# Optimization experiments

Hardware: AMD Instinct MI355X
Metric: run time of the kernel (lower is better)

The kernel has to match this reference:

```python
import jax, jax.numpy as jnp
import numpy as np
from functools import partial

DN = ('NCHW', 'OIHW', 'NCHW')

def _conv(x, w):
    # 'same' conv, stride 1, NCHW
    return jax.lax.conv_general_dilated(x, w, window_strides=(1, 1),
                                        padding='SAME', dimension_numbers=DN)

def setup_inputs() -> dict:
    key = jax.random.key(0)
    ks = jax.random.split(key, 5)
    B, T, Cin, Oh, H, Wd = 8, 16, 64, 64, 56, 56
    x = jax.random.normal(ks[0], (B, T, Cin, H, Wd), dtype=jnp.float32)
    h = jax.random.normal(ks[1], (B, Oh, H, Wd), dtype=jnp.float32)
    # xavier-uniform-ish init scale for 3x3 kernels
    def xavier(k, shape):
        fan_in = shape[1] * shape[2] * shape[3]
        fan_out = shape[0] * shape[2] * shape[3]
        a = float(np.sqrt(6.0 / (fan_in + fan_out)))
        return jax.random.uniform(k, shape, dtype=jnp.float32, minval=-a, maxval=a)
    W = xavier(ks[2], (3 * Oh, Cin, 3, 3))  # [Wz; Wr; Wc]
    U = xavier(ks[3], (2 * Oh, Oh, 3, 3))   # [Uz; Ur]
    C = xavier(ks[4], (Oh, Oh, 3, 3))       # Uc (on r*h)
    return {"x": x, "h": h, "W": W, "U": U, "C": C}

def reference(x, h, W, U, C):
    Oh = C.shape[0]
    xt_major = jnp.swapaxes(x, 0, 1)  # [T, B, Cin, H, W]

    def step(h, xt):
        wx = _conv(xt, W)             # [B, 3*Oh, H, W]
        uh = _conv(h, U)              # [B, 2*Oh, H, W]
        z = jax.nn.sigmoid(wx[:, :Oh] + uh[:, :Oh])            # update gate
        r = jax.nn.sigmoid(wx[:, Oh:2 * Oh] + uh[:, Oh:2 * Oh])  # reset gate
        h_tilde = jnp.tanh(wx[:, 2 * Oh:] + _conv(r * h, C))
        h_new = (1.0 - z) * h + z * h_tilde
        return h_new, h_new

    h_last, outs = jax.lax.scan(step, h, xt_major)
    return jnp.swapaxes(outs, 0, 1), h_last  # [B, T, Oh, H, W], [B, Oh, H, W]
```

## Files before the change

kernel.cpp:

```cpp
#include <hip/hip_runtime.h>
#include <math.h>


#define PIX 4224
#define PIMG 244992
#define BIMG ((size_t)8 * PIMG)
#define HL_OFF ((size_t)25690112)
#define SLOT 2176

typedef unsigned short u16;
typedef __attribute__((ext_vector_type(8))) __bf16 bf16x8;
typedef __attribute__((ext_vector_type(4))) float f32x4;

__device__ __forceinline__ float bf2f(u16 u) {
  unsigned v = ((unsigned)u) << 16;
  float f;
  __builtin_memcpy(&f, &v, 4);
  return f;
}
__device__ __forceinline__ u16 f2bf(float f) {
  unsigned u;
  __builtin_memcpy(&u, &f, 4);
  u = (u + 0x7FFFu + ((u >> 16) & 1u)) >> 16;
  return (u16)u;
}
__device__ __forceinline__ void gll16(const u16* g, u16* l) {
  __builtin_amdgcn_global_load_lds(
      (const __attribute__((address_space(1))) void*)g,
      (__attribute__((address_space(3))) void*)l, 16, 0, 0);
}

__device__ __forceinline__ void stage_row(const u16* img, int prow, int x0,
                                          u16* ring, int slot, int lane,
                                          int wv) {
  const u16* g = img + (size_t)prow * PIX + x0 * 64;
  u16* l = ring + slot * SLOT;
  gll16(g + wv * 512 + lane * 8, l + wv * 512);
  if (wv == 0 && lane < 16) gll16(g + 2048 + lane * 8, l + 2048);
}

__device__ __forceinline__ void loadB18(const u16* wr, int NCH,
                                        bf16x8 (&B)[6][3]) {
#pragma unroll
  for (int p = 0; p < 6; ++p) {
    const int ky = p >> 1, kc = p & 1;
#pragma unroll
    for (int kx = 0; kx < 3; ++kx)
      B[p][kx] = *(const bf16x8*)(wr + (size_t)((ky * 3 + kx) * NCH) * 64 +
                                  kc * 32);
  }
}

__device__ __forceinline__ void conv_unit(const u16* ring, int rcb,
                                          const bf16x8 (&B)[6][3],
                                          f32x4 (&acc)[2], int lane) {
#pragma unroll
  for (int p = 0; p < 6; ++p) {
    const int ky = p >> 1, kc = p & 1;
    const int slot = (rcb + ky) & 7;
    bf16x8 af[2][3];
#pragma unroll
    for (int mf = 0; mf < 2; ++mf)
#pragma unroll
      for (int kx = 0; kx < 3; ++kx) {
        const int pp = mf * 16 + (lane & 15) + kx;
        const int sl = (kc * 4 + (lane >> 4)) ^ (pp & 7);
        af[mf][kx] = *(const bf16x8*)(ring + slot * SLOT + pp * 64 + sl * 8);
      }
#pragma unroll
    for (int kx = 0; kx < 3; ++kx)
#pragma unroll
      for (int mf = 0; mf < 2; ++mf)
        acc[mf] = __builtin_amdgcn_mfma_f32_16x16x32_bf16(af[mf][kx], B[p][kx],
                                                          acc[mf], 0, 0, 0);
  }
}

#define UNIT_SYNC() \
  asm volatile("s_waitcnt vmcnt(0)" ::: "memory"); \
  __syncthreads();

__global__ __launch_bounds__(256) void wprep_k(const float* __restrict__ W,
                                               const float* __restrict__ U,
                                               const float* __restrict__ C,
                                               u16* __restrict__ wcat) {
  int i = blockIdx.x * 256 + threadIdx.x;
  if (i >= 221184) return;
  float v;
  if (i < 110592) {
    int plane = i / 12288, rem = i % 12288, o = rem / 64, ci = rem % 64;
    v = W[(size_t)(o * 64 + ci) * 9 + plane];
  } else if (i < 184320) {
    int j = i - 110592;
    int plane = j / 8192, rem = j % 8192, o = rem / 64, ci = rem % 64;
    v = U[(size_t)(o * 64 + ci) * 9 + plane];
  } else {
    int j = i - 184320;
    int plane = j / 4096, rem = j % 4096, o = rem / 64, ci = rem % 64;
    v = C[(size_t)(o * 64 + ci) * 9 + plane];
  }
  wcat[i] = f2bf(v);
}

__global__ __launch_bounds__(256) void hinit_k(const float* __restrict__ h,
                                               u16* __restrict__ hpad,
                                               float* __restrict__ hstate) {
  __shared__ float t[64][57];
  const int y = blockIdx.x, b = blockIdx.y;
  const int tid = threadIdx.x;
  for (int i = tid; i < 64 * 56; i += 256) {
    int ci = i / 56, xx = i % 56;
    t[ci][xx] = h[((size_t)(b * 64) + ci) * 3136 + y * 56 + xx];
  }
  __syncthreads();
  const size_t pb = (size_t)b * PIMG + (size_t)(y + 1) * PIX;
  const size_t sb = ((size_t)(b * 56) + y) * 64;
  for (int i = tid; i < 56 * 64; i += 256) {
    int px = i / 64, ci = i % 64;
    float v = t[ci][px];
    int gx = px + 1;
    hpad[pb + gx * 64 + (((ci >> 3) ^ (gx & 7)) << 3) + (ci & 7)] = f2bf(v);
    hstate[(sb + px) * 64 + ci] = v;
  }
}

__global__ __launch_bounds__(256) void xprep4_k(const float* __restrict__ x,
                                                u16* __restrict__ xring,
                                                int t0) {
  __shared__ float tt[64][57];
  const int y = blockIdx.x, b = blockIdx.y, t = t0 + blockIdx.z;
  const int tid = threadIdx.x;
  for (int i = tid; i < 64 * 56; i += 256) {
    int ci = i / 56, px = i % 56;
    tt[ci][px] = x[((size_t)(b * 16 + t) * 64 + ci) * 3136 + y * 56 + px];
  }
  __syncthreads();
  const size_t pb =
      (size_t)(t & 3) * BIMG + (size_t)b * PIMG + (size_t)(y + 1) * PIX;
  for (int i = tid; i < 56 * 64; i += 256) {
    int px = i / 64, ci = i % 64;
    int gx = px + 1;
    xring[pb + gx * 64 + (((ci >> 3) ^ (gx & 7)) << 3) + (ci & 7)] =
        f2bf(tt[ci][px]);
  }
}

__global__ __launch_bounds__(256, 3) void convW_k(const u16* __restrict__ xring,
                                                  const u16* __restrict__ wcat,
                                                  u16* __restrict__ wx) {
  __shared__ __align__(16) u16 ring[8 * SLOT];
  const int bid = blockIdx.x;
  const int ns = bid / 224;
  const int rem = bid % 224;
  const int b = rem & 7;
  const int r2 = rem >> 3;
  const int x0 = (r2 & 1) * 32;
  const int y0 = (r2 >> 1) * 4;
  const int lane = threadIdx.x & 63, wv = threadIdx.x >> 6;
  const int n0 = ns * 64 + wv * 16;

  const u16* wr = wcat + (size_t)(n0 + (lane & 15)) * 64 + (lane >> 4) * 8;
  bf16x8 B[6][3];
  loadB18(wr, 192, B);

  const u16* img0 = xring + (size_t)b * PIMG;

#pragma unroll
  for (int k = 0; k < 3; ++k)
    stage_row(img0, y0 + k, x0, ring, k, lane, wv);

  int S = 3;
#pragma unroll
  for (int u = 0; u < 16; ++u) {
    const int tt = u >> 2, yi = u & 3;
    UNIT_SYNC();
    const int tgt = (u + 1 < 16) ? (((u + 1) >> 2) * 6 + ((u + 1) & 3) + 2) : 2;
#pragma unroll
    for (; S <= tgt; ++S)
      stage_row(img0 + (size_t)(S / 6) * BIMG, y0 + S % 6, x0, ring, S & 7,
                lane, wv);

    f32x4 acc[2] = {{0.f, 0.f, 0.f, 0.f}, {0.f, 0.f, 0.f, 0.f}};
    conv_unit(ring, tt * 6 + yi, B, acc, lane);

    const int y = y0 + yi;
    const size_t rowb = ((size_t)(b * 4 + tt) * 56 + y) * 64;
    const int n = n0 + (lane & 15);
#pragma unroll
    for (int mf = 0; mf < 2; ++mf)
#pragma unroll
      for (int r = 0; r < 4; ++r) {
        const int px = x0 + mf * 16 + 4 * (lane >> 4) + r;
        wx[(rowb + px) * 192 + n] = f2bf(acc[mf][r]);
      }
  }
}

__global__ __launch_bounds__(256, 3) void convU_k(
    const u16* __restrict__ hpad, const u16* __restrict__ ucat,
    const u16* __restrict__ wx, _Float16* __restrict__ zbuf,
    u16* __restrict__ rhpad, int t) {
  __shared__ __align__(16) u16 ring[8 * SLOT];
  const int bid = blockIdx.x;
  const int ns = bid / 224;
  const int rem = bid % 224;
  const int b = rem & 7;
  const int r2 = rem >> 3;
  const int x0 = (r2 & 1) * 32;
  const int y0 = (r2 >> 1) * 4;
  const int lane = threadIdx.x & 63, wv = threadIdx.x >> 6;
  const int n0 = ns * 64 + wv * 16;

  const u16* wr = ucat + (size_t)(n0 + (lane & 15)) * 64 + (lane >> 4) * 8;
  bf16x8 B[6][3];
  loadB18(wr, 128, B);

  const u16* img = hpad + (size_t)b * PIMG;
#pragma unroll
  for (int k = 0; k < 3; ++k) stage_row(img, y0 + k, x0, ring, k, lane, wv);

  const int slott = t & 3;
  int S = 3;
#pragma unroll
  for (int u = 0; u < 4; ++u) {
    UNIT_SYNC();
    const int tgt = (u + 1 < 4) ? (u + 3) : 2;
#pragma unroll
    for (; S <= tgt; ++S)
      stage_row(img, y0 + S, x0, ring, S & 7, lane, wv);

    f32x4 acc[2] = {{0.f, 0.f, 0.f, 0.f}, {0.f, 0.f, 0.f, 0.f}};
    conv_unit(ring, u, B, acc, lane);

    const int y = y0 + u;
    const size_t wrowb = ((size_t)(b * 4 + slott) * 56 + y) * 64;
    const size_t rowb = ((size_t)(b * 56) + y) * 64;
    const int n = n0 + (lane & 15);
#pragma unroll
    for (int mf = 0; mf < 2; ++mf)
#pragma unroll
      for (int r = 0; r < 4; ++r) {
        const int px = x0 + mf * 16 + 4 * (lane >> 4) + r;
        if (px < 56) {
          const float a = bf2f(wx[(wrowb + px) * 192 + n]) + acc[mf][r];
          const float s = 1.f / (1.f + __expf(-a));
          if (ns == 0) {
            zbuf[(rowb + px) * 64 + n] = (_Float16)s;
          } else {
            const int ci = n - 64;
            const int cp = mf * 16 + 4 * (lane >> 4) + r + 1;
            const int slotc = (u + 1) & 7;
            const float hv =
                bf2f(ring[slotc * SLOT + cp * 64 +
                          (((ci >> 3) ^ (cp & 7)) << 3) + (ci & 7)]);
            const int gx = px + 1;
            rhpad[(size_t)b * PIMG + (size_t)(y + 1) * PIX + gx * 64 +
                  (((ci >> 3) ^ (gx & 7)) << 3) + (ci & 7)] = f2bf(s * hv);
          }
        }
      }
  }
}

__global__ __launch_bounds__(256, 3) void convC_k(
    const u16* __restrict__ rhpad, const u16* __restrict__ ccat,
    const u16* __restrict__ wx, const _Float16* __restrict__ zbuf,
    float* __restrict__ hstate, u16* __restrict__ hpad,
    float* __restrict__ out, int t) {
  __shared__ __align__(16) u16 ring[8 * SLOT];
  __shared__ float ldt[4][16][33];
  const int bid = blockIdx.x;
  const int b = bid & 7;
  const int r2 = bid >> 3;
  const int x0 = (r2 & 1) * 32;
  const int y0 = (r2 >> 1) * 2;
  const int lane = threadIdx.x & 63, wv = threadIdx.x >> 6;
  const int n0 = wv * 16;

  const u16* wr = ccat + (size_t)(n0 + (lane & 15)) * 64 + (lane >> 4) * 8;
  bf16x8 B[6][3];
  loadB18(wr, 64, B);

  const u16* img = rhpad + (size_t)b * PIMG;
#pragma unroll
  for (int k = 0; k < 3; ++k) stage_row(img, y0 + k, x0, ring, k, lane, wv);

  const int slott = t & 3;
#pragma unroll
  for (int u = 0; u < 2; ++u) {
    UNIT_SYNC();
    if (u == 0) stage_row(img, y0 + 3, x0, ring, 3, lane, wv);

    f32x4 acc[2] = {{0.f, 0.f, 0.f, 0.f}, {0.f, 0.f, 0.f, 0.f}};
    conv_unit(ring, u, B, acc, lane);

    const int y = y0 + u;
    const size_t wrowb = ((size_t)(b * 4 + slott) * 56 + y) * 64;
    const size_t rowb = ((size_t)(b * 56) + y) * 64;
    const int n = n0 + (lane & 15);
    float hnv[2][4];
#pragma unroll
    for (int mf = 0; mf < 2; ++mf)
#pragma unroll
      for (int r = 0; r < 4; ++r) {
        const int px = x0 + mf * 16 + 4 * (lane >> 4) + r;
        hnv[mf][r] = 0.f;
        if (px < 56) {
          const float a = bf2f(wx[(wrowb + px) * 192 + 128 + n]) + acc[mf][r];
          const float htil = tanhf(a);
          const float z = (float)zbuf[(rowb + px) * 64 + n];
          const float ho = hstate[(rowb + px) * 64 + n];
          const float hn = fmaf(z, htil - ho, ho);
          hstate[(rowb + px) * 64 + n] = hn;
          const int gx = px + 1;
          hpad[(size_t)b * PIMG + (size_t)(y + 1) * PIX + gx * 64 +
               (((n >> 3) ^ (gx & 7)) << 3) + (n & 7)] = f2bf(hn);
          hnv[mf][r] = hn;
        }
      }
    __syncthreads();
#pragma unroll
    for (int mf = 0; mf < 2; ++mf)
#pragma unroll
      for (int r = 0; r < 4; ++r)
        ldt[wv][lane & 15][mf * 16 + 4 * (lane >> 4) + r] = hnv[mf][r];
    __syncthreads();
    const int xl = lane & 31;
    const int px = x0 + xl;
    if (px < 56) {
#pragma unroll
      for (int cc = 0; cc < 8; ++cc) {
        const int ch = (lane >> 5) * 8 + cc;
        const float v = ldt[wv][ch][xl];
        out[(((size_t)(b * 16 + t)) * 64 + n0 + ch) * 3136 + y * 56 + px] = v;
        if (t == 15)
          out[HL_OFF + ((size_t)(b * 64) + n0 + ch) * 3136 + y * 56 + px] = v;
      }
    }
  }
}

extern "C" void kernel_launch(void* const* d_in, const int* in_sizes, int n_in,
                              void* d_out, int out_size, void* d_ws,
                              size_t ws_size, hipStream_t stream) {
  const float* x = (const float*)d_in[0];
  const float* h = (const float*)d_in[1];
  const float* W = (const float*)d_in[2];
  const float* U = (const float*)d_in[3];
  const float* C = (const float*)d_in[4];
  float* out = (float*)d_out;

  u16* ws_u = (u16*)d_ws;
  u16* xring = ws_u;
  u16* hpad = xring + 4 * BIMG;
  u16* rhpad = hpad + BIMG;
  u16* wcat = rhpad + BIMG;
  u16* wxr = wcat + 221184;
  _Float16* zbuf = (_Float16*)(wxr + 22020096);
  float* hstate = (float*)(zbuf + 1835008);

  hipMemsetAsync(d_ws, 0, (size_t)6 * BIMG * sizeof(u16), stream);
  wprep_k<<<864, 256, 0, stream>>>(W, U, C, wcat);
  hinit_k<<<dim3(56, 8), 256, 0, stream>>>(h, hpad, hstate);

  for (int g = 0; g < 4; ++g) {
    const int t0 = g * 4;
    xprep4_k<<<dim3(56, 8, 4), 256, 0, stream>>>(x, xring, t0);
    convW_k<<<672, 256, 0, stream>>>(xring, wcat, wxr);
    for (int tt = 0; tt < 4; ++tt) {
      const int t = t0 + tt;
      convU_k<<<448, 256, 0, stream>>>(hpad, wcat + 110592, wxr, zbuf, rhpad,
                                       t);
      convC_k<<<448, 256, 0, stream>>>(rhpad, wcat + 184320, wxr, zbuf, hstate,
                                       hpad, out, t);
    }
  }
}
```

Measured before the change: 883.9 us.

## Overlap next-step input conv and input prep with recurrent conv launches

The batched per-4-step input conv and input-prep launches are removed. Each recurrent step now appends extra blocks to its two launches. The U-conv launch also computes the W-conv for step t+1 into a double-buffered wx. The C-conv launch also converts the input frame for step t+2 into a double-buffered padded bf16 slot. The aim is to fill idle CUs while the small, latency-bound recurrent kernels run, and to drop separate launches and the 4-slot ring. The hidden-state copy is also stored as fp16 instead of fp32 to cut its traffic, which risks rounding error building up across the 16 recurrent steps.

Measured after the change: 813.7 us. 8.0% less time.

```diff
diff --git a/kernel.cpp b/kernel.cpp
--- a/kernel.cpp
+++ b/kernel.cpp
@@ -5,6 +5,7 @@
 #define PIX 4224
 #define PIMG 244992
 #define BIMG ((size_t)8 * PIMG)
+#define WXS ((size_t)5505024)
 #define HL_OFF ((size_t)25690112)
 #define SLOT 2176
 
@@ -79,6 +80,70 @@
 #define UNIT_SYNC() \
   asm volatile("s_waitcnt vmcnt(0)" ::: "memory"); \
   __syncthreads();
+
+__device__ __forceinline__ void do_convW(const u16* __restrict__ xslot,
+                                         const u16* __restrict__ wcat,
+                                         u16* __restrict__ wx, int id,
+                                         u16* ring) {
+  const int ns = id / 112;
+  const int rem = id % 112;
+  const int b = rem & 7;
+  const int v = rem >> 3;
+  const int x0 = (v & 1) * 32;
+  const int y0 = (v >> 1) * 8;
+  const int lane = threadIdx.x & 63, wv = threadIdx.x >> 6;
+  const int n0 = ns * 64 + wv * 16;
+
+  const u16* wr = wcat + (size_t)(n0 + (lane & 15)) * 64 + (lane >> 4) * 8;
+  bf16x8 B[6][3];
+  loadB18(wr, 192, B);
+
+  const u16* img = xslot + (size_t)b * PIMG;
+#pragma unroll
+  for (int k = 0; k < 3; ++k) stage_row(img, y0 + k, x0, ring, k, lane, wv);
+
+  int S = 3;
+#pragma unroll
+  for (int u = 0; u < 8; ++u) {
+    UNIT_SYNC();
+    const int tgt = (u + 1 < 8) ? (u + 3) : 2;
+#pragma unroll
+    for (; S <= tgt; ++S)
+      stage_row(img, y0 + S, x0, ring, S & 7, lane, wv);
+
+    f32x4 acc[2] = {{0.f, 0.f, 0.f, 0.f}, {0.f, 0.f, 0.f, 0.f}};
+    conv_unit(ring, u, B, acc, lane);
+
+    const int y = y0 + u;
+    const size_t rowb = ((size_t)(b * 56) + y) * 64;
+    const int n = n0 + (lane & 15);
+#pragma unroll
+    for (int mf = 0; mf < 2; ++mf)
+#pragma unroll
+      for (int r = 0; r < 4; ++r) {
+        const int px = x0 + mf * 16 + 4 * (lane >> 4) + r;
+        wx[(rowb + px) * 192 + n] = f2bf(acc[mf][r]);
+      }
+  }
+}
+
+__device__ __forceinline__ void xprep_row(const float* __restrict__ x,
+                                          u16* __restrict__ dst, int t, int b,
+                                          int y, float (*tx)[57]) {
+  const int tid = threadIdx.x;
+  for (int i = tid; i < 64 * 56; i += 256) {
+    int ci = i / 56, px = i % 56;
+    tx[ci][px] = x[((size_t)(b * 16 + t) * 64 + ci) * 3136 + y * 56 + px];
+  }
+  __syncthreads();
+  const size_t pb = (size_t)b * PIMG + (size_t)(y + 1) * PIX;
+  for (int i = tid; i < 56 * 64; i += 256) {
+    int px = i / 64, ci = i % 64;
+    int gx = px + 1;
+    dst[pb + gx * 64 + (((ci >> 3) ^ (gx & 7)) << 3) + (ci & 7)] =
+        f2bf(tx[ci][px]);
+  }
+}
 
 __global__ __launch_bounds__(256) void wprep_k(const float* __restrict__ W,
                                                const float* __restrict__ U,
@@ -104,7 +169,7 @@
 
 __global__ __launch_bounds__(256) void hinit_k(const float* __restrict__ h,
                                                u16* __restrict__ hpad,
-                                               float* __restrict__ hstate) {
+                                               _Float16* __restrict__ hstate) {
   __shared__ float t[64][57];
   const int y = blockIdx.x, b = blockIdx.y;
   const int tid = threadIdx.x;
@@ -120,36 +185,36 @@
     float v = t[ci][px];
     int gx = px + 1;
     hpad[pb + gx * 64 + (((ci >> 3) ^ (gx & 7)) << 3) + (ci & 7)] = f2bf(v);
-    hstate[(sb + px) * 64 + ci] = v;
-  }
-}
-
-__global__ __launch_bounds__(256) void xprep4_k(const float* __restrict__ x,
-                                                u16* __restrict__ xring,
-                                                int t0) {
+    hstate[(sb + px) * 64 + ci] = (_Float16)v;
+  }
+}
+
+__global__ __launch_bounds__(256) void xprep01_k(const float* __restrict__ x,
+                                                 u16* __restrict__ x0,
+                                                 u16* __restrict__ x1) {
   __shared__ float tt[64][57];
-  const int y = blockIdx.x, b = blockIdx.y, t = t0 + blockIdx.z;
-  const int tid = threadIdx.x;
-  for (int i = tid; i < 64 * 56; i += 256) {
-    int ci = i / 56, px = i % 56;
-    tt[ci][px] = x[((size_t)(b * 16 + t) * 64 + ci) * 3136 + y * 56 + px];
-  }
-  __syncthreads();
-  const size_t pb =
-      (size_t)(t & 3) * BIMG + (size_t)b * PIMG + (size_t)(y + 1) * PIX;
-  for (int i = tid; i < 56 * 64; i += 256) {
-    int px = i / 64, ci = i % 64;
-    int gx = px + 1;
-    xring[pb + gx * 64 + (((ci >> 3) ^ (gx & 7)) << 3) + (ci & 7)] =
-        f2bf(tt[ci][px]);
-  }
-}
-
-__global__ __launch_bounds__(256, 3) void convW_k(const u16* __restrict__ xring,
-                                                  const u16* __restrict__ wcat,
-                                                  u16* __restrict__ wx) {
+  const int t = blockIdx.y;
+  xprep_row(x, t ? x1 : x0, t, blockIdx.x & 7, blockIdx.x >> 3, tt);
+}
+
+__global__ __launch_bounds__(256, 3) void convW0_k(const u16* __restrict__ xs,
+                                                   const u16* __restrict__ wcat,
+                                                   u16* __restrict__ wx) {
+  __shared__ __align__(16) u16 ring[8 * SLOT];
+  do_convW(xs, wcat, wx, blockIdx.x, ring);
+}
+
+__global__ __launch_bounds__(256, 3) void convUW_k(
+    const u16* __restrict__ hpad, const u16* __restrict__ xpad_n,
+    const u16* __restrict__ wcat, const u16* __restrict__ wx_c,
+    u16* __restrict__ wx_n, _Float16* __restrict__ zbuf,
+    u16* __restrict__ rhpad) {
   __shared__ __align__(16) u16 ring[8 * SLOT];
   const int bid = blockIdx.x;
+  if (bid >= 448) {
+    do_convW(xpad_n, wcat, wx_n, bid - 448, ring);
+    return;
+  }
   const int ns = bid / 224;
   const int rem = bid % 224;
   const int b = rem & 7;
@@ -159,59 +224,8 @@
   const int lane = threadIdx.x & 63, wv = threadIdx.x >> 6;
   const int n0 = ns * 64 + wv * 16;
 
-  const u16* wr = wcat + (size_t)(n0 + (lane & 15)) * 64 + (lane >> 4) * 8;
-  bf16x8 B[6][3];
-  loadB18(wr, 192, B);
-
-  const u16* img0 = xring + (size_t)b * PIMG;
-
-#pragma unroll
-  for (int k = 0; k < 3; ++k)
-    stage_row(img0, y0 + k, x0, ring, k, lane, wv);
-
-  int S = 3;
-#pragma unroll
-  for (int u = 0; u < 16; ++u) {
-    const int tt = u >> 2, yi = u & 3;
-    UNIT_SYNC();
-    const int tgt = (u + 1 < 16) ? (((u + 1) >> 2) * 6 + ((u + 1) & 3) + 2) : 2;
-#pragma unroll
-    for (; S <= tgt; ++S)
-      stage_row(img0 + (size_t)(S / 6) * BIMG, y0 + S % 6, x0, ring, S & 7,
-                lane, wv);
-
-    f32x4 acc[2] = {{0.f, 0.f, 0.f, 0.f}, {0.f, 0.f, 0.f, 0.f}};
-    conv_unit(ring, tt * 6 + yi, B, acc, lane);
-
-    const int y = y0 + yi;
-    const size_t rowb = ((size_t)(b * 4 + tt) * 56 + y) * 64;
-    const int n = n0 + (lane & 15);
-#pragma unroll
-    for (int mf = 0; mf < 2; ++mf)
-#pragma unroll
-      for (int r = 0; r < 4; ++r) {
-        const int px = x0 + mf * 16 + 4 * (lane >> 4) + r;
-        wx[(rowb + px) * 192 + n] = f2bf(acc[mf][r]);
-      }
-  }
-}
-
-__global__ __launch_bounds__(256, 3) void convU_k(
-    const u16* __restrict__ hpad, const u16* __restrict__ ucat,
-    const u16* __restrict__ wx, _Float16* __restrict__ zbuf,
-    u16* __restrict__ rhpad, int t) {
-  __shared__ __align__(16) u16 ring[8 * SLOT];
-  const int bid = blockIdx.x;
-  const int ns = bid / 224;
-  const int rem = bid % 224;
-  const int b = rem & 7;
-  const int r2 = rem >> 3;
-  const int x0 = (r2 & 1) * 32;
-  const int y0 = (r2 >> 1) * 4;
-  const int lane = threadIdx.x & 63, wv = threadIdx.x >> 6;
-  const int n0 = ns * 64 + wv * 16;
-
-  const u16* wr = ucat + (size_t)(n0 + (lane & 15)) * 64 + (lane >> 4) * 8;
+  const u16* wr =
+      wcat + 110592 + (size_t)(n0 + (lane & 15)) * 64 + (lane >> 4) * 8;
   bf16x8 B[6][3];
   loadB18(wr, 128, B);
 
@@ -219,7 +233,6 @@
 #pragma unroll
   for (int k = 0; k < 3; ++k) stage_row(img, y0 + k, x0, ring, k, lane, wv);
 
-  const int slott = t & 3;
   int S = 3;
 #pragma unroll
   for (int u = 0; u < 4; ++u) {
@@ -233,7 +246,6 @@
     conv_unit(ring, u, B, acc, lane);
 
     const int y = y0 + u;
-    const size_t wrowb = ((size_t)(b * 4 + slott) * 56 + y) * 64;
     const size_t rowb = ((size_t)(b * 56) + y) * 64;
     const int n = n0 + (lane & 15);
 #pragma unroll
@@ -242,7 +254,7 @@
       for (int r = 0; r < 4; ++r) {
         const int px = x0 + mf * 16 + 4 * (lane >> 4) + r;
         if (px < 56) {
-          const float a = bf2f(wx[(wrowb + px) * 192 + n]) + acc[mf][r];
+          const float a = bf2f(wx_c[(rowb + px) * 192 + n]) + acc[mf][r];
           const float s = 1.f / (1.f + __expf(-a));
           if (ns == 0) {
             zbuf[(rowb + px) * 64 + n] = (_Float16)s;
@@ -262,14 +274,20 @@
   }
 }
 
-__global__ __launch_bounds__(256, 3) void convC_k(
-    const u16* __restrict__ rhpad, const u16* __restrict__ ccat,
-    const u16* __restrict__ wx, const _Float16* __restrict__ zbuf,
-    float* __restrict__ hstate, u16* __restrict__ hpad,
+__global__ __launch_bounds__(256, 3) void convCX_k(
+    const float* __restrict__ x, u16* __restrict__ xpad_w,
+    const u16* __restrict__ rhpad, const u16* __restrict__ wcat,
+    const u16* __restrict__ wx_c, const _Float16* __restrict__ zbuf,
+    _Float16* __restrict__ hstate, u16* __restrict__ hpad,
     float* __restrict__ out, int t) {
   __shared__ __align__(16) u16 ring[8 * SLOT];
   __shared__ float ldt[4][16][33];
   const int bid = blockIdx.x;
+  if (bid >= 448) {
+    const int id = bid - 448;
+    xprep_row(x, xpad_w, t + 2, id & 7, id >> 3, (float(*)[57])ring);
+    return;
+  }
   const int b = bid & 7;
   const int r2 = bid >> 3;
   const int x0 = (r2 & 1) * 32;
@@ -277,7 +295,8 @@
   const int lane = threadIdx.x & 63, wv = threadIdx.x >> 6;
   const int n0 = wv * 16;
 
-  const u16* wr = ccat + (size_t)(n0 + (lane & 15)) * 64 + (lane >> 4) * 8;
+  const u16* wr =
+      wcat + 184320 + (size_t)(n0 + (lane & 15)) * 64 + (lane >> 4) * 8;
   bf16x8 B[6][3];
   loadB18(wr, 64, B);
 
@@ -285,7 +304,6 @@
 #pragma unroll
   for (int k = 0; k < 3; ++k) stage_row(img, y0 + k, x0, ring, k, lane, wv);
 
-  const int slott = t & 3;
 #pragma unroll
   for (int u = 0; u < 2; ++u) {
     UNIT_SYNC();
@@ -295,7 +313,6 @@
     conv_unit(ring, u, B, acc, lane);
 
     const int y = y0 + u;
-    const size_t wrowb = ((size_t)(b * 4 + slott) * 56 + y) * 64;
     const size_t rowb = ((size_t)(b * 56) + y) * 64;
     const int n = n0 + (lane & 15);
     float hnv[2][4];
@@ -306,12 +323,12 @@
         const int px = x0 + mf * 16 + 4 * (lane >> 4) + r;
         hnv[mf][r] = 0.f;
         if (px < 56) {
-          const float a = bf2f(wx[(wrowb + px) * 192 + 128 + n]) + acc[mf][r];
+          const float a = bf2f(wx_c[(rowb + px) * 192 + 128 + n]) + acc[mf][r];
           const float htil = tanhf(a);
           const float z = (float)zbuf[(rowb + px) * 64 + n];
-          const float ho = hstate[(rowb + px) * 64 + n];
+          const float ho = (float)hstate[(rowb + px) * 64 + n];
           const float hn = fmaf(z, htil - ho, ho);
-          hstate[(rowb + px) * 64 + n] = hn;
+          hstate[(rowb + px) * 64 + n] = (_Float16)hn;
           const int gx = px + 1;
           hpad[(size_t)b * PIMG + (size_t)(y + 1) * PIX + gx * 64 +
                (((n >> 3) ^ (gx & 7)) << 3) + (n & 7)] = f2bf(hn);
@@ -351,28 +368,31 @@
   float* out = (float*)d_out;
 
   u16* ws_u = (u16*)d_ws;
-  u16* xring = ws_u;
-  u16* hpad = xring + 4 * BIMG;
+  u16* xpad = ws_u;
+  u16* hpad = xpad + 2 * BIMG;
   u16* rhpad = hpad + BIMG;
   u16* wcat = rhpad + BIMG;
   u16* wxr = wcat + 221184;
-  _Float16* zbuf = (_Float16*)(wxr + 22020096);
-  float* hstate = (float*)(zbuf + 1835008);
-
-  hipMemsetAsync(d_ws, 0, (size_t)6 * BIMG * sizeof(u16), stream);
+  _Float16* zbuf = (_Float16*)(wxr + 2 * WXS);
+  _Float16* hstate = zbuf + 1835008;
+
+  hipMemsetAsync(d_ws, 0, (size_t)4 * BIMG * sizeof(u16), stream);
   wprep_k<<<864, 256, 0, stream>>>(W, U, C, wcat);
   hinit_k<<<dim3(56, 8), 256, 0, stream>>>(h, hpad, hstate);
-
-  for (int g = 0; g < 4; ++g) {
-    const int t0 = g * 4;
-    xprep4_k<<<dim3(56, 8, 4), 256, 0, stream>>>(x, xring, t0);
-    convW_k<<<672, 256, 0, stream>>>(xring, wcat, wxr);
-    for (int tt = 0; tt < 4; ++tt) {
-      const int t = t0 + tt;
-      convU_k<<<448, 256, 0, stream>>>(hpad, wcat + 110592, wxr, zbuf, rhpad,
-                                       t);
-      convC_k<<<448, 256, 0, stream>>>(rhpad, wcat + 184320, wxr, zbuf, hstate,
-                                       hpad, out, t);
-    }
-  }
-}
+  xprep01_k<<<dim3(448, 2), 256, 0, stream>>>(x, xpad, xpad + BIMG);
+  convW0_k<<<336, 256, 0, stream>>>(xpad, wcat, wxr);
+
+  for (int t = 0; t < 16; ++t) {
+    u16* xn = xpad + (size_t)((t + 1) & 1) * BIMG;
+    u16* xw = xpad + (size_t)(t & 1) * BIMG;
+    const u16* wxc = wxr + (size_t)(t & 1) * WXS;
+    u16* wxn = wxr + (size_t)((t + 1) & 1) * WXS;
+
+    const int nbA = 448 + ((t < 15) ? 336 : 0);
+    convUW_k<<<nbA, 256, 0, stream>>>(hpad, xn, wcat, wxc, wxn, zbuf, rhpad);
+
+    const int nbB = 448 + ((t < 14) ? 448 : 0);
+    convCX_k<<<nbB, 256, 0, stream>>>(x, xw, rhpad, wcat, wxc, zbuf, hstate,
+                                      hpad, out, t);
+  }
+}
```
